# Optimization experiments

Measured on AMD Instinct MI355X. Metric: run time of the kernel, lower is better.

The kernel has to match this reference:

```python
import jax, jax.numpy as jnp
import numpy as np

SIZE_IN = 4096
SIZE_OUT = 4096
BATCH = 4096


def setup_inputs() -> dict:
    key = jax.random.key(0)
    k1, k2, k3, k4, k5, k6 = jax.random.split(key, 6)
    mu_in = jax.random.normal(k1, (BATCH, SIZE_IN), dtype=jnp.float32)
    sigma_in = jax.random.uniform(k2, (BATCH, SIZE_IN), dtype=jnp.float32)
    # parameters, initialized as in the torch module
    w_mu = 5e-05 * jax.random.normal(k3, (SIZE_IN, SIZE_OUT), dtype=jnp.float32)
    w_sigma = jax.random.uniform(k4, (SIZE_IN * SIZE_OUT,), dtype=jnp.float32,
                                 minval=-12.0, maxval=-2.2)
    b_mu = 5e-05 * jax.random.normal(k5, (SIZE_OUT,), dtype=jnp.float32)
    b_sigma = jax.random.uniform(k6, (SIZE_OUT,), dtype=jnp.float32,
                                 minval=-12.0, maxval=-10.0)
    return {"mu_in": mu_in, "sigma_in": sigma_in, "w_mu": w_mu,
            "w_sigma": w_sigma, "b_mu": b_mu, "b_sigma": b_sigma}


def reference(mu_in, sigma_in, w_mu, w_sigma, b_mu, b_sigma):
    # mean path: mu_out[b,o] = sum_i mu_in[b,i] * w_mu[i,o] + b_mu[o]
    mu_out = jnp.einsum('bi,io->bo', mu_in, w_mu) + b_mu
    # variance path: x diag(softplus(w_sigma)) x^T, per output feature.
    # Equivalent to (mu_in^2) @ softplus(w_sigma).reshape(size_in, size_out),
    # avoiding the quadratic diag_embed + bmm materialization.
    sigma_w = jax.nn.softplus(w_sigma).reshape(SIZE_IN, SIZE_OUT)
    Sigma_out = jnp.einsum('bi,io->bo', mu_in * mu_in, sigma_w) + jax.nn.softplus(b_sigma)
    # KL loss, verbatim from the torch code
    sp = jax.nn.softplus(w_sigma)
    term1 = SIZE_IN * jnp.log(sp)
    term2 = jnp.sum(jnp.abs(w_mu))
    term3 = SIZE_IN * sp
    kl_loss = -0.5 * jnp.mean(term1 - term2 - term3)
    return (mu_out, Sigma_out, kl_loss)
```

## Files before the change

### kernel.cpp

```cpp
#include <hip/hip_runtime.h>
#include <hip/hip_bf16.h>
#include <math.h>

#define M_BATCH   4096
#define K_IN      4096
#define N_OUT     4096
#define NELEM     16777216

typedef __bf16 bf16;
typedef bf16  bf16x8 __attribute__((ext_vector_type(8)));
typedef float f32x4  __attribute__((ext_vector_type(4)));

__device__ __forceinline__ float softplus_fast(float x) {
    if (x > 15.f) return x;
    const float e = __expf(x);
    if (e < 0.0883f)
        return e * (1.f + e * (-0.5f + e * 0.3333333f));
    return __logf(1.f + e);
}

__device__ __forceinline__ unsigned short f2bf_bits(float x) {
    bf16 b = (bf16)x;
    return __builtin_bit_cast(unsigned short, b);
}

__device__ __forceinline__ void gload_lds16(const void* g, void* l) {
    __builtin_amdgcn_global_load_lds(
        (__attribute__((address_space(1))) void*)g,
        (__attribute__((address_space(3))) void*)l,
        16, 0, 0);
}

__global__ __launch_bounds__(256) void prep_a(const float4* __restrict__ mu,
                                              ushort4* __restrict__ A,
                                              ushort4* __restrict__ A2) {
    const int i = blockIdx.x * 256 + threadIdx.x;
    const float4 v = mu[i];
    ushort4 a, a2;
    a.x  = f2bf_bits(v.x);       a.y  = f2bf_bits(v.y);
    a.z  = f2bf_bits(v.z);       a.w  = f2bf_bits(v.w);
    a2.x = f2bf_bits(v.x * v.x); a2.y = f2bf_bits(v.y * v.y);
    a2.z = f2bf_bits(v.z * v.z); a2.w = f2bf_bits(v.w * v.w);
    A[i]  = a;
    A2[i] = a2;
}

__global__ __launch_bounds__(256) void prep_w(const float* __restrict__ wmu,
                                              const float* __restrict__ wsg,
                                              bf16* __restrict__ Wmu_t,
                                              bf16* __restrict__ Wsg_t,
                                              float* __restrict__ partials) {
    __shared__ bf16 tmu[64][65];
    __shared__ bf16 tsg[64][65];
    __shared__ float red[256];

    const int t  = threadIdx.x;
    const int ti = blockIdx.y;
    const int tj = blockIdx.x;
    const int r  = t >> 4;
    const int c4 = (t & 15) << 2;

    float s_abs = 0.f, s_sp = 0.f, s_log = 0.f;

    for (int rr = 0; rr < 64; rr += 16) {
        const int row = rr + r;
        const size_t goff = (size_t)(ti * 64 + row) * N_OUT + tj * 64 + c4;
        const float4 vm = *(const float4*)(wmu + goff);
        const float4 vs = *(const float4*)(wsg + goff);
        const float sp0 = softplus_fast(vs.x), sp1 = softplus_fast(vs.y);
        const float sp2 = softplus_fast(vs.z), sp3 = softplus_fast(vs.w);
        s_abs += fabsf(vm.x) + fabsf(vm.y) + fabsf(vm.z) + fabsf(vm.w);
        s_sp  += sp0 + sp1 + sp2 + sp3;
        s_log += __logf(sp0) + __logf(sp1) + __logf(sp2) + __logf(sp3);
        tmu[row][c4 + 0] = (bf16)vm.x; tmu[row][c4 + 1] = (bf16)vm.y;
        tmu[row][c4 + 2] = (bf16)vm.z; tmu[row][c4 + 3] = (bf16)vm.w;
        tsg[row][c4 + 0] = (bf16)sp0;  tsg[row][c4 + 1] = (bf16)sp1;
        tsg[row][c4 + 2] = (bf16)sp2;  tsg[row][c4 + 3] = (bf16)sp3;
    }
    __syncthreads();

    for (int cc = 0; cc < 64; cc += 16) {
        const int j  = cc + r;
        const int i0 = c4;
        ushort4 om, os;
        om.x = __builtin_bit_cast(unsigned short, tmu[i0 + 0][j]);
        om.y = __builtin_bit_cast(unsigned short, tmu[i0 + 1][j]);
        om.z = __builtin_bit_cast(unsigned short, tmu[i0 + 2][j]);
        om.w = __builtin_bit_cast(unsigned short, tmu[i0 + 3][j]);
        os.x = __builtin_bit_cast(unsigned short, tsg[i0 + 0][j]);
        os.y = __builtin_bit_cast(unsigned short, tsg[i0 + 1][j]);
        os.z = __builtin_bit_cast(unsigned short, tsg[i0 + 2][j]);
        os.w = __builtin_bit_cast(unsigned short, tsg[i0 + 3][j]);
        const size_t o = (size_t)(tj * 64 + j) * K_IN + ti * 64 + i0;
        *(ushort4*)(Wmu_t + o) = om;
        *(ushort4*)(Wsg_t + o) = os;
    }

    const int bid = blockIdx.y * 64 + blockIdx.x;
    float vals[3] = { s_log, s_sp, s_abs };
    for (int v = 0; v < 3; v++) {
        __syncthreads();
        red[t] = vals[v];
        __syncthreads();
        for (int s = 128; s > 0; s >>= 1) {
            if (t < s) red[t] += red[t + s];
            __syncthreads();
        }
        if (t == 0) partials[v * 4096 + bid] = red[0];
    }
}

#define MFMA_BF16 __builtin_amdgcn_mfma_f32_16x16x32_bf16

__global__ __launch_bounds__(512, 2) void gemm_bf16(
    const bf16* __restrict__ A1,  const bf16* __restrict__ Bt1,
    const float* __restrict__ bias1, float* __restrict__ C1,
    const bf16* __restrict__ A2_, const bf16* __restrict__ Bt2,
    const float* __restrict__ bias2, float* __restrict__ C2) {

    __shared__ bf16 As[2 * 256 * 64];
    __shared__ bf16 Bs[2 * 256 * 64];

    const int z = blockIdx.z;
    const bf16*  A    = z ? A2_   : A1;
    const bf16*  Bt   = z ? Bt2   : Bt1;
    const float* bias = z ? bias2 : bias1;
    float*       C    = z ? C2    : C1;

    const int t = threadIdx.x;
    const int id  = blockIdx.y * 16 + blockIdx.x;
    const int swz = (id & 7) * 32 + (id >> 3);
    const int rowBase = (swz >> 4) << 8;
    const int colBase = (swz & 15) << 8;

    const int srow   = t >> 3;
    const int schunk = (t & 7) ^ (srow & 7);
    const char* aG = (const char*)(A  + (size_t)(rowBase + srow) * K_IN + schunk * 8);
    const char* bG = (const char*)(Bt + (size_t)(colBase + srow) * K_IN + schunk * 8);
    char* aL = (char*)As + t * 16;
    char* bL = (char*)Bs + t * 16;

#define STAGE_A(kt, h, par) do {                                               \
        const size_t kb_ = (size_t)((kt) & 63) << 7;                           \
        gload_lds16(aG + kb_ + (size_t)(h) * (128 * K_IN * 2),                 \
                    aL + ((par) << 15) + ((h) << 14));                         \
        gload_lds16(aG + kb_ + (size_t)(h) * (128 * K_IN * 2) + 64 * K_IN * 2, \
                    aL + ((par) << 15) + ((h) << 14) + 8192);                  \
    } while (0)
#define STAGE_B(kt, h, par) do {                                               \
        const size_t kb_ = (size_t)((kt) & 63) << 7;                           \
        gload_lds16(bG + kb_ + (size_t)(h) * (128 * K_IN * 2),                 \
                    bL + ((par) << 15) + ((h) << 14));                         \
        gload_lds16(bG + kb_ + (size_t)(h) * (128 * K_IN * 2) + 64 * K_IN * 2, \
                    bL + ((par) << 15) + ((h) << 14) + 8192);                  \
    } while (0)

    const int lane = t & 63;
    const int wave = t >> 6;
    const int wr = wave >> 2;
    const int wc = wave & 3;
    const int frow = lane & 15;
    const int blk0 = (lane >> 4) ^ (lane & 7);
    const int c0 = blk0 << 4;
    const int c1 = (blk0 ^ 4) << 4;
    const char* aRd = (const char*)As + ((wr << 7) + frow) * 128;
    const char* bRd = (const char*)Bs + ((wc << 6) + frow) * 128;

#define DS_A(par, fi, ck) (*(const bf16x8*)(aRd + ((par) << 15) + ((fi) << 11) + (ck)))
#define DS_B(par, n,  ck) (*(const bf16x8*)(bRd + ((par) << 15) + ((n)  << 11) + (ck)))

    const f32x4 zero = { 0.f, 0.f, 0.f, 0.f };
    f32x4 acc[8][4];
#pragma unroll
    for (int m = 0; m < 8; ++m)
#pragma unroll
        for (int n = 0; n < 4; ++n) acc[m][n] = zero;

#define PHASE(par, q, STAGE_STMT, VM) do {                                        \
        if ((q) == 0) {                                                           \
            _Pragma("unroll")                                                     \
            for (int n = 0; n < 4; ++n) {                                         \
                bfrag[n][0] = DS_B(par, n, c0);                                   \
                bfrag[n][1] = DS_B(par, n, c1);                                   \
            }                                                                     \
        }                                                                         \
        const bf16x8 a0k0 = DS_A(par, (q) * 2 + 0, c0);                           \
        const bf16x8 a0k1 = DS_A(par, (q) * 2 + 0, c1);                           \
        const bf16x8 a1k0 = DS_A(par, (q) * 2 + 1, c0);                           \
        const bf16x8 a1k1 = DS_A(par, (q) * 2 + 1, c1);                           \
        STAGE_STMT;                                                               \
        if (VM) asm volatile("s_waitcnt vmcnt(4)" ::: "memory");                  \
        __builtin_amdgcn_sched_barrier(0);                                        \
        __builtin_amdgcn_s_barrier();                                             \
        __builtin_amdgcn_sched_barrier(0);                                        \
        __builtin_amdgcn_s_setprio(1);                                            \
        _Pragma("unroll")                                                         \
        for (int n = 0; n < 4; ++n) {                                             \
            acc[(q)*2+0][n] = MFMA_BF16(a0k0, bfrag[n][0], acc[(q)*2+0][n],0,0,0);\
            acc[(q)*2+0][n] = MFMA_BF16(a0k1, bfrag[n][1], acc[(q)*2+0][n],0,0,0);\
            acc[(q)*2+1][n] = MFMA_BF16(a1k0, bfrag[n][0], acc[(q)*2+1][n],0,0,0);\
            acc[(q)*2+1][n] = MFMA_BF16(a1k1, bfrag[n][1], acc[(q)*2+1][n],0,0,0);\
        }                                                                         \
        __builtin_amdgcn_s_setprio(0);                                            \
        __builtin_amdgcn_sched_barrier(0);                                        \
        __builtin_amdgcn_s_barrier();                                             \
        __builtin_amdgcn_sched_barrier(0);                                        \
    } while (0)

    STAGE_A(0, 0, 0); STAGE_A(0, 1, 0);
    STAGE_B(0, 0, 0); STAGE_B(0, 1, 0);
    STAGE_A(1, 0, 1); STAGE_A(1, 1, 1);
    STAGE_B(1, 0, 1); STAGE_B(1, 1, 1);
    asm volatile("s_waitcnt vmcnt(8)" ::: "memory");
    __builtin_amdgcn_sched_barrier(0);
    __builtin_amdgcn_s_barrier();
    __builtin_amdgcn_sched_barrier(0);

    for (int i = 0; i < 32; ++i) {
        const int kA1 = 2 * i + 1;
        const int kB0 = 2 * i + 2;
        const int kA0 = 2 * i + 2;
        const int kB1 = 2 * i + 3;
        {
            bf16x8 bfrag[4][2];
            PHASE(0, 0, STAGE_A(kA1, 0, 1), 0);
            PHASE(0, 1, STAGE_A(kA1, 1, 1), 0);
            PHASE(0, 2, STAGE_B(kB0, 0, 0), 0);
            PHASE(0, 3, STAGE_B(kB0, 1, 0), 1);
        }
        {
            bf16x8 bfrag[4][2];
            PHASE(1, 0, STAGE_A(kA0, 0, 0), 0);
            PHASE(1, 1, STAGE_A(kA0, 1, 0), 0);
            PHASE(1, 2, STAGE_B(kB1, 0, 1), 0);
            PHASE(1, 3, STAGE_B(kB1, 1, 1), 1);
        }
    }

    asm volatile("s_waitcnt vmcnt(0)" ::: "memory");

    const int r0 = (lane >> 4) << 2;
    const int ccol = colBase + (wc << 6) + (lane & 15);
#pragma unroll
    for (int n = 0; n < 4; ++n) {
        const int c = ccol + n * 16;
        float b = bias[c];
        if (z) b = softplus_fast(b);
#pragma unroll
        for (int m = 0; m < 8; ++m) {
            const int rbase = rowBase + (wr << 7) + (m << 4) + r0;
#pragma unroll
            for (int reg = 0; reg < 4; ++reg)
                C[(size_t)(rbase + reg) * N_OUT + c] = acc[m][n][reg] + b;
        }
    }
#undef STAGE_A
#undef STAGE_B
#undef DS_A
#undef DS_B
#undef PHASE
}

__global__ __launch_bounds__(256) void kl_finish(const float* __restrict__ partials,
                                                 const int n,
                                                 float* __restrict__ out) {
    __shared__ double red[256];
    const int t = threadIdx.x;
    double sums[3];
    for (int v = 0; v < 3; v++) {
        double a = 0.0;
        for (int i = t; i < n; i += 256) a += (double)partials[v * n + i];
        red[t] = a;
        __syncthreads();
        for (int s = 128; s > 0; s >>= 1) {
            if (t < s) red[t] += red[t + s];
            __syncthreads();
        }
        sums[v] = red[0];
        __syncthreads();
    }
    if (t == 0) {
        const double mean_log = sums[0] / 16777216.0;
        const double mean_sp  = sums[1] / 16777216.0;
        const double kl = -0.5 * (4096.0 * mean_log - sums[2] - 4096.0 * mean_sp);
        out[0] = (float)kl;
    }
}

__global__ void fb_partials(const float* __restrict__ wmu,
                            const float* __restrict__ wsg,
                            float* __restrict__ partials) {
    __shared__ float red[256];
    const int t = threadIdx.x;
    float s_abs = 0.f, s_sp = 0.f, s_log = 0.f;
    for (int i = blockIdx.x * 256 + t; i < NELEM; i += 1024 * 256) {
        s_abs += fabsf(wmu[i]);
        const float sp = softplus_fast(wsg[i]);
        s_sp += sp;
        s_log += __logf(sp);
    }
    float vals[3] = { s_log, s_sp, s_abs };
    for (int v = 0; v < 3; v++) {
        __syncthreads();
        red[t] = vals[v];
        __syncthreads();
        for (int s = 128; s > 0; s >>= 1) {
            if (t < s) red[t] += red[t + s];
            __syncthreads();
        }
        if (t == 0) partials[v * 1024 + blockIdx.x] = red[0];
    }
}

__global__ void fb_gemm(const float* __restrict__ A,
                        const float* __restrict__ Wm,
                        const float* __restrict__ Ws,
                        const float* __restrict__ bmu,
                        const float* __restrict__ bsg,
                        float* __restrict__ Cmu,
                        float* __restrict__ Csg) {
    __shared__ float As_[16][17], Bm[16][17], Bs_[16][17];
    const int tx = threadIdx.x, ty = threadIdx.y;
    const int row = blockIdx.y * 16 + ty;
    const int col = blockIdx.x * 16 + tx;
    float am = 0.f, as = 0.f;
    for (int k0 = 0; k0 < K_IN; k0 += 16) {
        As_[ty][tx] = A[(size_t)row * K_IN + k0 + tx];
        Bm[ty][tx]  = Wm[(size_t)(k0 + ty) * N_OUT + col];
        Bs_[ty][tx] = softplus_fast(Ws[(size_t)(k0 + ty) * N_OUT + col]);
        __syncthreads();
#pragma unroll
        for (int kk = 0; kk < 16; kk++) {
            const float av = As_[ty][kk];
            am += av * Bm[kk][tx];
            as += av * av * Bs_[kk][tx];
        }
        __syncthreads();
    }
    Cmu[(size_t)row * N_OUT + col] = am + bmu[col];
    Csg[(size_t)row * N_OUT + col] = as + softplus_fast(bsg[col]);
}

extern "C" void kernel_launch(void* const* d_in, const int* in_sizes, int n_in,
                              void* d_out, int out_size, void* d_ws, size_t ws_size,
                              hipStream_t stream) {
    const float* mu_in   = (const float*)d_in[0];
    const float* w_mu    = (const float*)d_in[2];
    const float* w_sigma = (const float*)d_in[3];
    const float* b_mu    = (const float*)d_in[4];
    const float* b_sigma = (const float*)d_in[5];

    float* out_mu  = (float*)d_out;
    float* out_sig = out_mu + (size_t)NELEM;
    float* out_kl  = out_mu + 2 * (size_t)NELEM;

    const size_t mat  = (size_t)NELEM;
    const size_t need = mat * 2 * 4  + 3 * 4096 * sizeof(float);

    if (ws_size >= need) {
        bf16* A      = (bf16*)d_ws;
        bf16* A2     = A + mat;
        bf16* Wmu_t  = A2 + mat;
        bf16* Wsg_t  = Wmu_t + mat;
        float* parts = (float*)(Wsg_t + mat);

        prep_a<<<NELEM / 4 / 256, 256, 0, stream>>>(
            (const float4*)mu_in, (ushort4*)A, (ushort4*)A2);
        prep_w<<<dim3(64, 64), 256, 0, stream>>>(
            w_mu, w_sigma, Wmu_t, Wsg_t, parts);
        gemm_bf16<<<dim3(16, 16, 2), 512, 0, stream>>>(
            A, Wmu_t, b_mu, out_mu, A2, Wsg_t, b_sigma, out_sig);
        kl_finish<<<1, 256, 0, stream>>>(parts, 4096, out_kl);
    } else {
        float* parts = (float*)d_ws;
        fb_partials<<<1024, 256, 0, stream>>>(w_mu, w_sigma, parts);
        fb_gemm<<<dim3(256, 256), dim3(16, 16), 0, stream>>>(
            mu_in, w_mu, w_sigma, b_mu, b_sigma, out_mu, out_sig);
        kl_finish<<<1, 256, 0, stream>>>(parts, 1024, out_kl);
    }
}
```

Measured before the change: 587.0 us.

## Software-pipeline LDS fragment reads ahead of MFMAs and remap tiles per XCD

```diff
diff --git a/kernel.cpp b/kernel.cpp
--- a/kernel.cpp
+++ b/kernel.cpp
@@ -128,10 +128,10 @@
     float*       C    = z ? C2    : C1;
 
     const int t = threadIdx.x;
-    const int id  = blockIdx.y * 16 + blockIdx.x;
-    const int swz = (id & 7) * 32 + (id >> 3);
-    const int rowBase = (swz >> 4) << 8;
-    const int colBase = (swz & 15) << 8;
+    const int id   = blockIdx.y * 16 + blockIdx.x;
+    const int xcd  = id & 7, cc_ = id >> 3;
+    const int rowBase = (((xcd >> 1) << 2) + (cc_ >> 3)) << 8;
+    const int colBase = (((xcd & 1) << 3) + (cc_ & 7)) << 8;
 
     const int srow   = t >> 3;
     const int schunk = (t & 7) ^ (srow & 7);
@@ -169,6 +169,56 @@
 #define DS_A(par, fi, ck) (*(const bf16x8*)(aRd + ((par) << 15) + ((fi) << 11) + (ck)))
 #define DS_B(par, n,  ck) (*(const bf16x8*)(bRd + ((par) << 15) + ((n)  << 11) + (ck)))
 
+#define READ_A2(set, par, fi) do {                                             \
+        aF[set][0] = DS_A(par, (fi),     c0);                                  \
+        aF[set][1] = DS_A(par, (fi),     c1);                                  \
+        aF[set][2] = DS_A(par, (fi) + 1, c0);                                  \
+        aF[set][3] = DS_A(par, (fi) + 1, c1);                                  \
+    } while (0)
+#define READ_B1(par, n) do {                                                   \
+        bfrag[n][0] = DS_B(par, n, c0);                                        \
+        bfrag[n][1] = DS_B(par, n, c1);                                        \
+    } while (0)
+
+#define MFMA_PAIR(q, set, n) do {                                              \
+        acc[(q)*2+0][n] = MFMA_BF16(aF[set][0], bfrag[n][0], acc[(q)*2+0][n],0,0,0); \
+        acc[(q)*2+0][n] = MFMA_BF16(aF[set][1], bfrag[n][1], acc[(q)*2+0][n],0,0,0); \
+        acc[(q)*2+1][n] = MFMA_BF16(aF[set][2], bfrag[n][0], acc[(q)*2+1][n],0,0,0); \
+        acc[(q)*2+1][n] = MFMA_BF16(aF[set][3], bfrag[n][1], acc[(q)*2+1][n],0,0,0); \
+    } while (0)
+
+#define PRE(STAGE_STMT, VM) do {                                               \
+        STAGE_STMT;                                                            \
+        if (VM) asm volatile("s_waitcnt vmcnt(4)" ::: "memory");               \
+        __builtin_amdgcn_sched_barrier(0);                                     \
+        __builtin_amdgcn_s_barrier();                                          \
+        __builtin_amdgcn_sched_barrier(0);                                     \
+    } while (0)
+
+#define MREG(q, set, RDAHEAD) do {                                             \
+        RDAHEAD;                                                               \
+        __builtin_amdgcn_s_setprio(1);                                         \
+        MFMA_PAIR(q, set, 0); MFMA_PAIR(q, set, 1);                            \
+        MFMA_PAIR(q, set, 2); MFMA_PAIR(q, set, 3);                            \
+        __builtin_amdgcn_s_setprio(0);                                         \
+        __builtin_amdgcn_sched_barrier(0);                                     \
+        __builtin_amdgcn_s_barrier();                                          \
+        __builtin_amdgcn_sched_barrier(0);                                     \
+    } while (0)
+
+#define MREG_Q3(set, parN) do {                                                \
+        READ_A2(set ^ 1, parN, 0);                                             \
+        __builtin_amdgcn_s_setprio(1);                                         \
+        MFMA_PAIR(3, set, 0); MFMA_PAIR(3, set, 1);                            \
+        READ_B1(parN, 0); READ_B1(parN, 1);                                    \
+        MFMA_PAIR(3, set, 2); MFMA_PAIR(3, set, 3);                            \
+        READ_B1(parN, 2); READ_B1(parN, 3);                                    \
+        __builtin_amdgcn_s_setprio(0);                                         \
+        __builtin_amdgcn_sched_barrier(0);                                     \
+        __builtin_amdgcn_s_barrier();                                          \
+        __builtin_amdgcn_sched_barrier(0);                                     \
+    } while (0)
+
     const f32x4 zero = { 0.f, 0.f, 0.f, 0.f };
     f32x4 acc[8][4];
 #pragma unroll
@@ -176,36 +226,8 @@
 #pragma unroll
         for (int n = 0; n < 4; ++n) acc[m][n] = zero;
 
-#define PHASE(par, q, STAGE_STMT, VM) do {                                        \
-        if ((q) == 0) {                                                           \
-            _Pragma("unroll")                                                     \
-            for (int n = 0; n < 4; ++n) {                                         \
-                bfrag[n][0] = DS_B(par, n, c0);                                   \
-                bfrag[n][1] = DS_B(par, n, c1);                                   \
-            }                                                                     \
-        }                                                                         \
-        const bf16x8 a0k0 = DS_A(par, (q) * 2 + 0, c0);                           \
-        const bf16x8 a0k1 = DS_A(par, (q) * 2 + 0, c1);                           \
-        const bf16x8 a1k0 = DS_A(par, (q) * 2 + 1, c0);                           \
-        const bf16x8 a1k1 = DS_A(par, (q) * 2 + 1, c1);                           \
-        STAGE_STMT;                                                               \
-        if (VM) asm volatile("s_waitcnt vmcnt(4)" ::: "memory");                  \
-        __builtin_amdgcn_sched_barrier(0);                                        \
-        __builtin_amdgcn_s_barrier();                                             \
-        __builtin_amdgcn_sched_barrier(0);                                        \
-        __builtin_amdgcn_s_setprio(1);                                            \
-        _Pragma("unroll")                                                         \
-        for (int n = 0; n < 4; ++n) {                                             \
-            acc[(q)*2+0][n] = MFMA_BF16(a0k0, bfrag[n][0], acc[(q)*2+0][n],0,0,0);\
-            acc[(q)*2+0][n] = MFMA_BF16(a0k1, bfrag[n][1], acc[(q)*2+0][n],0,0,0);\
-            acc[(q)*2+1][n] = MFMA_BF16(a1k0, bfrag[n][0], acc[(q)*2+1][n],0,0,0);\
-            acc[(q)*2+1][n] = MFMA_BF16(a1k1, bfrag[n][1], acc[(q)*2+1][n],0,0,0);\
-        }                                                                         \
-        __builtin_amdgcn_s_setprio(0);                                            \
-        __builtin_amdgcn_sched_barrier(0);                                        \
-        __builtin_amdgcn_s_barrier();                                             \
-        __builtin_amdgcn_sched_barrier(0);                                        \
-    } while (0)
+    bf16x8 aF[2][4];
+    bf16x8 bfrag[4][2];
 
     STAGE_A(0, 0, 0); STAGE_A(0, 1, 0);
     STAGE_B(0, 0, 0); STAGE_B(0, 1, 0);
@@ -216,28 +238,26 @@
     __builtin_amdgcn_s_barrier();
     __builtin_amdgcn_sched_barrier(0);
 
+    READ_A2(0, 0, 0);
+    READ_B1(0, 0); READ_B1(0, 1); READ_B1(0, 2); READ_B1(0, 3);
+
     for (int i = 0; i < 32; ++i) {
         const int kA1 = 2 * i + 1;
         const int kB0 = 2 * i + 2;
         const int kA0 = 2 * i + 2;
         const int kB1 = 2 * i + 3;
-        {
-            bf16x8 bfrag[4][2];
-            PHASE(0, 0, STAGE_A(kA1, 0, 1), 0);
-            PHASE(0, 1, STAGE_A(kA1, 1, 1), 0);
-            PHASE(0, 2, STAGE_B(kB0, 0, 0), 0);
-            PHASE(0, 3, STAGE_B(kB0, 1, 0), 1);
-        }
-        {
-            bf16x8 bfrag[4][2];
-            PHASE(1, 0, STAGE_A(kA0, 0, 0), 0);
-            PHASE(1, 1, STAGE_A(kA0, 1, 0), 0);
-            PHASE(1, 2, STAGE_B(kB1, 0, 1), 0);
-            PHASE(1, 3, STAGE_B(kB1, 1, 1), 1);
-        }
+        PRE(STAGE_A(kA1, 0, 1), 0);  MREG(0, 0, READ_A2(1, 0, 2));
+        PRE(STAGE_A(kA1, 1, 1), 0);  MREG(1, 1, READ_A2(0, 0, 4));
+        PRE(STAGE_B(kB0, 0, 0), 0);  MREG(2, 0, READ_A2(1, 0, 6));
+        PRE(STAGE_B(kB0, 1, 0), 1);  MREG_Q3(1, 1);
+        PRE(STAGE_A(kA0, 0, 0), 0);  MREG(0, 0, READ_A2(1, 1, 2));
+        PRE(STAGE_A(kA0, 1, 0), 0);  MREG(1, 1, READ_A2(0, 1, 4));
+        PRE(STAGE_B(kB1, 0, 1), 0);  MREG(2, 0, READ_A2(1, 1, 6));
+        PRE(STAGE_B(kB1, 1, 1), 1);  MREG_Q3(1, 0);
     }
 
     asm volatile("s_waitcnt vmcnt(0)" ::: "memory");
+    asm volatile("" :: "v"(aF[0][0]), "v"(bfrag[0][0]));
 
     const int r0 = (lane >> 4) << 2;
     const int ccol = colBase + (wc << 6) + (lane & 15);
@@ -258,7 +278,12 @@
 #undef STAGE_B
 #undef DS_A
 #undef DS_B
-#undef PHASE
+#undef READ_A2
+#undef READ_B1
+#undef MFMA_PAIR
+#undef PRE
+#undef MREG
+#undef MREG_Q3
 }
 
 __global__ __launch_bounds__(256) void kl_finish(const float* __restrict__ partials,
```

Result: slower. 630.0 us (+7.3%).
